# Kernel optimization log

Hardware: AMD Instinct MI355X
Metric: run time of the kernel (lower is better)

## Reference

```python
import jax, jax.numpy as jnp
import numpy as np
from jax.scipy.special import logsumexp

B, N = 256, 65536
NEG_INF = jnp.float32(-1e30)  # acts as -inf for logsumexp, keeps grads finite


def setup_inputs() -> dict:
    key = jax.random.key(0)
    k1, k2 = jax.random.split(key)
    sim = jax.random.uniform(k1, (B, N), dtype=jnp.float32)
    label = jax.random.uniform(k2, (B, N), dtype=jnp.float32)
    return {"sim": sim, "label": label}


def _ranking_loss(sim, label):
    m = 0.2
    gamma = 64.0
    delta_p = 1.0 - m  # 0.8
    delta_n = m        # 0.2

    pos_mask = label > 0.5
    neg_mask = label < 0.25

    # ---- positives: logit_p = -relu(0.8 - sim).detach() * (sim - 0.8) * gamma ----
    alpha_p = jax.lax.stop_gradient(jnp.maximum(0.8 - sim, 0.0))
    logit_p = -alpha_p * (sim - delta_p) * gamma
    lse_p = logsumexp(jnp.where(pos_mask, logit_p, NEG_INF), axis=1)
    # torch fallback: no positives -> logit_p = [0.0], logsumexp == 0
    lse_p = jnp.where(pos_mask.any(axis=1), lse_p, 0.0)

    # ---- negatives: if >20 negatives, keep only top-10 largest sims ----
    alpha_n_all = jax.lax.stop_gradient(jnp.maximum(sim - 0.2, 0.0))
    logit_n_all = alpha_n_all * (sim - delta_n) * gamma
    lse_n_all = logsumexp(jnp.where(neg_mask, logit_n_all, NEG_INF), axis=1)

    neg_sim_masked = jnp.where(neg_mask, sim, NEG_INF)
    top_v, _ = jax.lax.top_k(neg_sim_masked, 10)  # [B, 10]
    alpha_n_top = jax.lax.stop_gradient(jnp.maximum(top_v - 0.2, 0.0))
    logit_n_top = alpha_n_top * (top_v - delta_n) * gamma
    lse_n_top = logsumexp(logit_n_top, axis=1)

    n_neg = neg_mask.sum(axis=1)
    lse_n = jnp.where(n_neg > 20, lse_n_top, lse_n_all)

    loss_loc = jax.nn.softplus(lse_n + lse_p).sum()
    return loss_loc / sim.shape[0]  # reduction='mean'


def reference(sim, label):
    return _ranking_loss(sim, label)
```

## Files before the change

kernel.cpp:

```cpp
#include <hip/hip_runtime.h>
#include <cmath>

#define NEG_INF (-1.0e30f)

static constexpr int B = 256;
static constexpr int N = 65536;
static constexpr int THREADS = 256;
static constexpr float C_OFF = 40.96f;
static constexpr float PAD = 0.2f;

typedef float f32x4 __attribute__((ext_vector_type(4)));

__device__ __forceinline__ float wave_sum_f(float v) {
#pragma unroll
  for (int off = 32; off >= 1; off >>= 1) v += __shfl_xor(v, off, 64);
  return v;
}

__device__ __forceinline__ void merge_lists_shfl(float t[16], int off) {
  float b[16];
#pragma unroll
  for (int i = 0; i < 16; ++i) b[i] = __shfl_xor(t[i], off, 64);
  float c[16];
#pragma unroll
  for (int i = 0; i < 16; ++i) c[i] = fmaxf(t[i], b[15 - i]);
#pragma unroll
  for (int s = 8; s >= 1; s >>= 1) {
#pragma unroll
    for (int i = 0; i < 16; ++i) {
      if ((i & s) == 0) {
        float lo = c[i], hi = c[i + s];
        c[i] = fmaxf(lo, hi);
        c[i + s] = fminf(lo, hi);
      }
    }
  }
#pragma unroll
  for (int i = 0; i < 16; ++i) t[i] = c[i];
}

__device__ __forceinline__ void merge_lists_local(float a[16], const float b[16]) {
  float c[16];
#pragma unroll
  for (int i = 0; i < 16; ++i) c[i] = fmaxf(a[i], b[15 - i]);
#pragma unroll
  for (int s = 8; s >= 1; s >>= 1) {
#pragma unroll
    for (int i = 0; i < 16; ++i) {
      if ((i & s) == 0) {
        float lo = c[i], hi = c[i + s];
        c[i] = fmaxf(lo, hi);
        c[i + s] = fminf(lo, hi);
      }
    }
  }
#pragma unroll
  for (int i = 0; i < 16; ++i) a[i] = c[i];
}

__device__ __forceinline__ void process_elem(float s, float l, float& s_p,
                                             float& s_n, int& nn, float t[10]) {
  const bool pos = l > 0.5f;
  const bool neg = l < 0.25f;
  float d = pos ? (0.8f - s) : (s - 0.2f);
  float r = fmaxf(d, 0.f);
  float arg = __builtin_fmaf(64.f * r, r, -C_OFF);
  float e = __expf(arg);
  if (pos) s_p += e;
  if (neg) s_n += e;
  nn += (int)__popcll(__ballot(neg));
  float se = neg ? s : PAD;
  if (se > t[9]) {
    float prev = t[0];
    t[0] = fmaxf(t[0], se);
#pragma unroll
    for (int i = 1; i < 10; ++i) {
      float cur = t[i];
      t[i] = __builtin_amdgcn_fmed3f(se, prev, cur);
      prev = cur;
    }
  }
}

template <int SPLIT>
__global__ void __launch_bounds__(THREADS, 4) ranking_partial_kernel(
    const float* __restrict__ sim, const float* __restrict__ label,
    float* __restrict__ ws_sp, float* __restrict__ ws_sn,
    int* __restrict__ ws_cnt, float* __restrict__ ws_top) {
  const int blk = blockIdx.x;
  const int row = blk / SPLIT;
  const int part = blk % SPLIT;
  const int tid = threadIdx.x;
  const size_t base4 = (size_t)row * (N / 4) + (size_t)part * (N / (4 * SPLIT));
  const f32x4* sim4 = reinterpret_cast<const f32x4*>(sim) + base4;
  const f32x4* lab4 = reinterpret_cast<const f32x4*>(label) + base4;

  float s_p = 0.f, s_n = 0.f;
  int nn = 0;
  float t[10];
#pragma unroll
  for (int i = 0; i < 10; ++i) t[i] = PAD;

  constexpr int ITER = N / 4 / THREADS / SPLIT;
  constexpr int PF = (ITER > 8) ? 8 : ITER;

#pragma unroll
  for (int base = 0; base < ITER; base += PF) {
    f32x4 sv[PF], lv[PF];
#pragma unroll
    for (int j = 0; j < PF; ++j) {
      sv[j] = sim4[(base + j) * THREADS + tid];
      lv[j] = lab4[(base + j) * THREADS + tid];
    }
#pragma unroll
    for (int j = 0; j < PF; ++j) {
      asm volatile("" : "+v"(sv[j][0]), "+v"(sv[j][1]), "+v"(sv[j][2]), "+v"(sv[j][3]));
      asm volatile("" : "+v"(lv[j][0]), "+v"(lv[j][1]), "+v"(lv[j][2]), "+v"(lv[j][3]));
    }
    __builtin_amdgcn_sched_barrier(0);
#pragma unroll
    for (int j = 0; j < PF; ++j) {
      process_elem(sv[j][0], lv[j][0], s_p, s_n, nn, t);
      process_elem(sv[j][1], lv[j][1], s_p, s_n, nn, t);
      process_elem(sv[j][2], lv[j][2], s_p, s_n, nn, t);
      process_elem(sv[j][3], lv[j][3], s_p, s_n, nn, t);
    }
  }

  float tl[16];
#pragma unroll
  for (int i = 0; i < 10; ++i) tl[i] = t[i];
#pragma unroll
  for (int i = 10; i < 16; ++i) tl[i] = PAD;

  s_p = wave_sum_f(s_p);
  s_n = wave_sum_f(s_n);
#pragma unroll
  for (int off = 1; off < 64; off <<= 1) merge_lists_shfl(tl, off);

  __shared__ float ls_p[4], ls_n[4];
  __shared__ int ls_c[4];
  __shared__ float ltop[4][16];
  const int wave = tid >> 6, lane = tid & 63;
  if (lane == 0) {
    ls_p[wave] = s_p;
    ls_n[wave] = s_n;
    ls_c[wave] = nn;
#pragma unroll
    for (int i = 0; i < 16; ++i) ltop[wave][i] = tl[i];
  }
  __syncthreads();

  if (wave == 0) {
    float m[16];
    if (lane < 4) {
#pragma unroll
      for (int i = 0; i < 16; ++i) m[i] = ltop[lane][i];
    } else {
#pragma unroll
      for (int i = 0; i < 16; ++i) m[i] = PAD;
    }
    merge_lists_shfl(m, 1);
    merge_lists_shfl(m, 2);

    float sp = (lane < 4) ? ls_p[lane] : 0.f;
    float sn = (lane < 4) ? ls_n[lane] : 0.f;
    int cn = (lane < 4) ? ls_c[lane] : 0;
    sp = wave_sum_f(sp);
    sn = wave_sum_f(sn);
#pragma unroll
    for (int off = 32; off >= 1; off >>= 1) cn += __shfl_xor(cn, off, 64);

    if (lane == 0) {
      ws_sp[blk] = sp;
      ws_sn[blk] = sn;
      ws_cnt[blk] = cn;
#pragma unroll
      for (int i = 0; i < 16; ++i) ws_top[blk * 16 + i] = m[i];
    }
  }
}

template <int SPLIT>
__global__ void __launch_bounds__(256) combine_kernel(
    const float* __restrict__ ws_sp, const float* __restrict__ ws_sn,
    const int* __restrict__ ws_cnt, const float* __restrict__ ws_top,
    float* __restrict__ out) {
  const int r = threadIdx.x;
  const int p0 = r * SPLIT;

  float a[16];
#pragma unroll
  for (int i = 0; i < 16; ++i) a[i] = ws_top[p0 * 16 + i];
#pragma unroll
  for (int k = 1; k < SPLIT; ++k) {
    float b[16];
#pragma unroll
    for (int i = 0; i < 16; ++i) b[i] = ws_top[(p0 + k) * 16 + i];
    merge_lists_local(a, b);
  }

  float sp = 0.f, sn = 0.f;
  int cn = 0;
#pragma unroll
  for (int k = 0; k < SPLIT; ++k) {
    sp += ws_sp[p0 + k];
    sn += ws_sn[p0 + k];
    cn += ws_cnt[p0 + k];
  }

  float lse_p = (sp > 0.f) ? (C_OFF + __logf(sp)) : 0.f;
  float lse_n_all = (sn > 0.f) ? (C_OFF + __logf(sn)) : NEG_INF;

  float mx = NEG_INF;
  float lg[10];
#pragma unroll
  for (int i = 0; i < 10; ++i) {
    float v = a[i];
    float al = fmaxf(v - 0.2f, 0.f);
    float lo = al * (v - 0.2f) * 64.f;
    lg[i] = lo;
    mx = fmaxf(mx, lo);
  }
  float ss = 0.f;
#pragma unroll
  for (int i = 0; i < 10; ++i) ss += __expf(lg[i] - mx);
  float lse_n_top = mx + __logf(ss);

  float lse_n = (cn > 20) ? lse_n_top : lse_n_all;
  float x = lse_n + lse_p;
  float loss = fmaxf(x, 0.f) + log1pf(__expf(-fabsf(x)));

  float v = wave_sum_f(loss);
  __shared__ float wsh[4];
  if ((r & 63) == 0) wsh[r >> 6] = v;
  __syncthreads();
  if (r == 0) out[0] = (wsh[0] + wsh[1] + wsh[2] + wsh[3]) * (1.0f / 256.0f);
}

template <int SPLIT>
static void launch_all(const float* sim, const float* label, float* out,
                       float* wsf, hipStream_t stream) {
  constexpr int P = B * SPLIT;
  float* ws_sp = wsf;
  float* ws_sn = wsf + P;
  float* ws_top = wsf + 2 * P;
  int* ws_cnt = (int*)(wsf + 2 * P + P * 16);
  ranking_partial_kernel<SPLIT><<<dim3(P), dim3(THREADS), 0, stream>>>(
      sim, label, ws_sp, ws_sn, ws_cnt, ws_top);
  combine_kernel<SPLIT><<<dim3(1), dim3(256), 0, stream>>>(ws_sp, ws_sn, ws_cnt,
                                                           ws_top, out);
}

extern "C" void kernel_launch(void* const* d_in, const int* in_sizes, int n_in,
                              void* d_out, int out_size, void* d_ws, size_t ws_size,
                              hipStream_t stream) {
  const float* sim = (const float*)d_in[0];
  const float* label = (const float*)d_in[1];
  float* out = (float*)d_out;
  float* wsf = (float*)d_ws;

  auto need = [](int split) { return (size_t)B * split * 19 * sizeof(float); };
  if (ws_size >= need(8)) {
    launch_all<8>(sim, label, out, wsf, stream);
  } else if (ws_size >= need(4)) {
    launch_all<4>(sim, label, out, wsf, stream);
  } else {
    launch_all<2>(sim, label, out, wsf, stream);
  }
}
```

Before: 155.7 us.

## Stage input loads into LDS with double-buffered global_load_lds pipeline

```diff
diff --git a/kernel.cpp b/kernel.cpp
--- a/kernel.cpp
+++ b/kernel.cpp
@@ -8,8 +8,15 @@
 static constexpr int THREADS = 256;
 static constexpr float C_OFF = 40.96f;
 static constexpr float PAD = 0.2f;
+static constexpr int CH = 2;
 
 typedef float f32x4 __attribute__((ext_vector_type(4)));
+
+typedef __attribute__((address_space(3))) void as3_void;
+typedef __attribute__((address_space(1))) const void as1_void;
+__device__ __forceinline__ void stage16(const f32x4* g, const f32x4* l) {
+  __builtin_amdgcn_global_load_lds((as1_void*)g, (as3_void*)l, 16, 0, 0);
+}
 
 __device__ __forceinline__ float wave_sum_f(float v) {
 #pragma unroll
@@ -82,6 +89,15 @@
   }
 }
 
+__device__ __forceinline__ void process_vec4(const f32x4& sv, const f32x4& lv,
+                                             float& s_p, float& s_n, int& nn,
+                                             float t[10]) {
+  process_elem(sv[0], lv[0], s_p, s_n, nn, t);
+  process_elem(sv[1], lv[1], s_p, s_n, nn, t);
+  process_elem(sv[2], lv[2], s_p, s_n, nn, t);
+  process_elem(sv[3], lv[3], s_p, s_n, nn, t);
+}
+
 template <int SPLIT>
 __global__ void __launch_bounds__(THREADS, 4) ranking_partial_kernel(
     const float* __restrict__ sim, const float* __restrict__ label,
@@ -95,35 +111,47 @@
   const f32x4* sim4 = reinterpret_cast<const f32x4*>(sim) + base4;
   const f32x4* lab4 = reinterpret_cast<const f32x4*>(label) + base4;
 
+  __shared__ f32x4 lds_s[2][CH * THREADS];
+  __shared__ f32x4 lds_l[2][CH * THREADS];
+
+  constexpr int ITER = N / 4 / THREADS / SPLIT;
+  constexpr int NC = ITER / CH;
+  static_assert(ITER % CH == 0, "chunking assumes ITER % CH == 0");
+
+  const int wbase = tid & ~63;
+
+  auto stage = [&](int buf, int c) {
+#pragma unroll
+    for (int j = 0; j < CH; ++j) {
+      const int idx = j * THREADS + wbase;
+      const int gidx = c * CH * THREADS + j * THREADS + tid;
+      stage16(sim4 + gidx, &lds_s[buf][idx]);
+      stage16(lab4 + gidx, &lds_l[buf][idx]);
+    }
+  };
+
   float s_p = 0.f, s_n = 0.f;
   int nn = 0;
   float t[10];
 #pragma unroll
   for (int i = 0; i < 10; ++i) t[i] = PAD;
 
-  constexpr int ITER = N / 4 / THREADS / SPLIT;
-  constexpr int PF = (ITER > 8) ? 8 : ITER;
-
-#pragma unroll
-  for (int base = 0; base < ITER; base += PF) {
-    f32x4 sv[PF], lv[PF];
-#pragma unroll
-    for (int j = 0; j < PF; ++j) {
-      sv[j] = sim4[(base + j) * THREADS + tid];
-      lv[j] = lab4[(base + j) * THREADS + tid];
-    }
-#pragma unroll
-    for (int j = 0; j < PF; ++j) {
-      asm volatile("" : "+v"(sv[j][0]), "+v"(sv[j][1]), "+v"(sv[j][2]), "+v"(sv[j][3]));
-      asm volatile("" : "+v"(lv[j][0]), "+v"(lv[j][1]), "+v"(lv[j][2]), "+v"(lv[j][3]));
+  stage(0, 0);
+#pragma unroll 1
+  for (int c = 0; c < NC; ++c) {
+    if (c + 1 < NC) {
+      asm volatile("s_waitcnt lgkmcnt(0)" ::: "memory");
+      stage((c + 1) & 1, c + 1);
+      asm volatile("s_waitcnt vmcnt(4)" ::: "memory");
+    } else {
+      asm volatile("s_waitcnt vmcnt(0)" ::: "memory");
     }
     __builtin_amdgcn_sched_barrier(0);
 #pragma unroll
-    for (int j = 0; j < PF; ++j) {
-      process_elem(sv[j][0], lv[j][0], s_p, s_n, nn, t);
-      process_elem(sv[j][1], lv[j][1], s_p, s_n, nn, t);
-      process_elem(sv[j][2], lv[j][2], s_p, s_n, nn, t);
-      process_elem(sv[j][3], lv[j][3], s_p, s_n, nn, t);
+    for (int j = 0; j < CH; ++j) {
+      f32x4 sv = lds_s[c & 1][j * THREADS + tid];
+      f32x4 lv = lds_l[c & 1][j * THREADS + tid];
+      process_vec4(sv, lv, s_p, s_n, nn, t);
     }
   }
 
@@ -176,7 +204,7 @@
       ws_sn[blk] = sn;
       ws_cnt[blk] = cn;
 #pragma unroll
-      for (int i = 0; i < 16; ++i) ws_top[blk * 16 + i] = m[i];
+      for (int i = 0; i < 10; ++i) ws_top[blk * 10 + i] = m[i];
     }
   }
 }
@@ -191,12 +219,16 @@
 
   float a[16];
 #pragma unroll
-  for (int i = 0; i < 16; ++i) a[i] = ws_top[p0 * 16 + i];
+  for (int i = 0; i < 10; ++i) a[i] = ws_top[p0 * 10 + i];
+#pragma unroll
+  for (int i = 10; i < 16; ++i) a[i] = PAD;
 #pragma unroll
   for (int k = 1; k < SPLIT; ++k) {
     float b[16];
 #pragma unroll
-    for (int i = 0; i < 16; ++i) b[i] = ws_top[(p0 + k) * 16 + i];
+    for (int i = 0; i < 10; ++i) b[i] = ws_top[(p0 + k) * 10 + i];
+#pragma unroll
+    for (int i = 10; i < 16; ++i) b[i] = PAD;
     merge_lists_local(a, b);
   }
 
@@ -245,7 +277,7 @@
   float* ws_sp = wsf;
   float* ws_sn = wsf + P;
   float* ws_top = wsf + 2 * P;
-  int* ws_cnt = (int*)(wsf + 2 * P + P * 16);
+  int* ws_cnt = (int*)(wsf + 2 * P + P * 10);
   ranking_partial_kernel<SPLIT><<<dim3(P), dim3(THREADS), 0, stream>>>(
       sim, label, ws_sp, ws_sn, ws_cnt, ws_top);
   combine_kernel<SPLIT><<<dim3(1), dim3(256), 0, stream>>>(ws_sp, ws_sn, ws_cnt,
@@ -260,7 +292,7 @@
   float* out = (float*)d_out;
   float* wsf = (float*)d_ws;
 
-  auto need = [](int split) { return (size_t)B * split * 19 * sizeof(float); };
+  auto need = [](int split) { return (size_t)B * split * 13 * sizeof(float); };
   if (ws_size >= need(8)) {
     launch_all<8>(sim, label, out, wsf, stream);
   } else if (ws_size >= need(4)) {
```

Result: no change. 155.6 us (-0.0%).
